# Kernel tuning notes

Measured on AMD Instinct MI355X. Metric: run time of the kernel, lower is better.

## Reference

```python
import jax, jax.numpy as jnp
import numpy as np

N_USERS = 100000
N_ITEMS = 50000
N_EDGES = 1000000
D = 64


def setup_inputs() -> dict:
    key = jax.random.key(0)
    ks = jax.random.split(key, 8)
    return {
        "h_user": jax.random.normal(ks[0], (N_USERS, D), dtype=jnp.float32),
        "h_item": jax.random.normal(ks[1], (N_ITEMS, D), dtype=jnp.float32),
        "buy_src": jax.random.randint(ks[2], (N_EDGES,), 0, N_USERS),
        "buy_dst": jax.random.randint(ks[3], (N_EDGES,), 0, N_ITEMS),
        "w_buy": jax.random.uniform(ks[4], (N_EDGES,), dtype=jnp.float32),
        "bought_src": jax.random.randint(ks[5], (N_EDGES,), 0, N_ITEMS),
        "bought_dst": jax.random.randint(ks[6], (N_EDGES,), 0, N_USERS),
        "w_bought": jax.random.uniform(ks[7], (N_EDGES,), dtype=jnp.float32),
    }


def reference(h_user, h_item, buy_src, buy_dst, w_buy, bought_src, bought_dst, w_bought):
    # 'buy' etype: user -> item. message m = h_user[src] * w, reduce sum at item dst.
    msg_buy = h_user[buy_src] * w_buy[:, None]  # [E, D]
    new_item = jax.ops.segment_sum(msg_buy, buy_dst, num_segments=h_item.shape[0])
    # 'bought' etype: item -> user. message m = h_item[src] * w, reduce sum at user dst.
    msg_bought = h_item[bought_src] * w_bought[:, None]  # [E, D]
    new_user = jax.ops.segment_sum(msg_bought, bought_dst, num_segments=h_user.shape[0])
    # multi_update_all cross-reducer 'mean' is identity here: each ntype is written
    # by exactly one etype, so mean over one contribution == the sum itself.
    return (new_user, new_item)
```

## Files before the change

kernel.cpp:

```cpp
#include <hip/hip_runtime.h>


#define DIM 64

#define RB2     64
#define CAP_I   2048
#define CAP_U   1024
#define NBLK_FC 256

#define RB   128
#define CAP  4096
#define NBLK 256

__global__ void zero_u32(unsigned* __restrict__ p, int n) {
    int i = blockIdx.x * blockDim.x + threadIdx.x;
    if (i < n) p[i] = 0u;
}

__global__ void zero_f32(float4* __restrict__ out, long long n4) {
    long long i = (long long)blockIdx.x * blockDim.x + threadIdx.x;
    const long long stride = (long long)gridDim.x * blockDim.x;
    for (; i < n4; i += stride) out[i] = make_float4(0.f, 0.f, 0.f, 0.f);
}

__global__ void conv_bf16(const float4* __restrict__ in, uint4* __restrict__ out,
                          long long n8) {
    long long i = (long long)blockIdx.x * blockDim.x + threadIdx.x;
    const long long stride = (long long)gridDim.x * blockDim.x;
    for (; i < n8; i += stride) {
        const float4 a = in[2 * i];
        const float4 b = in[2 * i + 1];
        const unsigned* pa = (const unsigned*)&a;
        const unsigned* pb = (const unsigned*)&b;
        unsigned r[8];
        #pragma unroll
        for (int k = 0; k < 4; ++k) {
            unsigned u = pa[k];
            r[k] = (u + 0x7FFFu + ((u >> 16) & 1u)) >> 16;
        }
        #pragma unroll
        for (int k = 0; k < 4; ++k) {
            unsigned u = pb[k];
            r[4 + k] = (u + 0x7FFFu + ((u >> 16) & 1u)) >> 16;
        }
        uint4 o;
        o.x = r[0] | (r[1] << 16);
        o.y = r[2] | (r[3] << 16);
        o.z = r[4] | (r[5] << 16);
        o.w = r[6] | (r[7] << 16);
        out[i] = o;
    }
}

__global__ void scatter_both(const float* __restrict__ h_user,
                             const float* __restrict__ h_item,
                             const int* __restrict__ buy_src,
                             const int* __restrict__ buy_dst,
                             const float* __restrict__ w_buy,
                             const int* __restrict__ bought_src,
                             const int* __restrict__ bought_dst,
                             const float* __restrict__ w_bought,
                             float* __restrict__ new_user,
                             float* __restrict__ new_item,
                             int n_buy, int n_total) {
    const int lane = threadIdx.x & 63;
    const int waves_per_block = blockDim.x >> 6;
    int wid = blockIdx.x * waves_per_block + (threadIdx.x >> 6);
    const int nwaves = gridDim.x * waves_per_block;
    for (int e = wid; e < n_total; e += nwaves) {
        const float* h; const int* srcp; const int* dstp; const float* wp;
        float* outp; int idx;
        if (e < n_buy) { h = h_user; srcp = buy_src; dstp = buy_dst; wp = w_buy; outp = new_item; idx = e; }
        else { h = h_item; srcp = bought_src; dstp = bought_dst; wp = w_bought; outp = new_user; idx = e - n_buy; }
        const int s = srcp[idx];
        const int d = dstp[idx];
        const float weight = wp[idx];
        const float v = h[(long long)s * DIM + lane] * weight;
        atomicAdd(outp + (long long)d * DIM + lane, v);
    }
}


__global__ __launch_bounds__(512) void k3_fc(
        const int* __restrict__ buy_src, const int* __restrict__ buy_dst,
        const float* __restrict__ w_buy,
        const int* __restrict__ bought_src, const int* __restrict__ bought_dst,
        const float* __restrict__ w_bought,
        unsigned* __restrict__ cur, uint2* __restrict__ pay,
        int n_buy, int n_total, int g_item, int G, int chunk) {
    extern __shared__ unsigned sh[];
    for (int g = threadIdx.x; g < G; g += blockDim.x) sh[g] = 0u;
    __syncthreads();
    const int start = blockIdx.x * chunk;
    const int end = (start + chunk < n_total) ? start + chunk : n_total;
    const int step = blockDim.x;

    int i = start + threadIdx.x;
    for (; i + 7 * step < end; i += 8 * step) {
        int g[8];
        #pragma unroll
        for (int u = 0; u < 8; ++u) {
            const int ii = i + u * step;
            g[u] = (ii < n_buy) ? (buy_dst[ii] >> 6)
                                : (g_item + (bought_dst[ii - n_buy] >> 6));
        }
        #pragma unroll
        for (int u = 0; u < 8; ++u) atomicAdd(&sh[g[u]], 1u);
    }
    for (; i < end; i += step) {
        const int g = (i < n_buy) ? (buy_dst[i] >> 6)
                                  : (g_item + (bought_dst[i - n_buy] >> 6));
        atomicAdd(&sh[g], 1u);
    }
    __syncthreads();

    for (int g = threadIdx.x; g < G; g += blockDim.x) {
        const unsigned c = sh[g];
        sh[g] = c ? atomicAdd(&cur[g], c) : 0u;
    }
    __syncthreads();

    i = start + threadIdx.x;
    for (; i + 3 * step < end; i += 4 * step) {
        int srcv[4], dstv[4]; float wv[4]; int g[4];
        #pragma unroll
        for (int u = 0; u < 4; ++u) {
            const int ii = i + u * step;
            if (ii < n_buy) {
                srcv[u] = buy_src[ii]; dstv[u] = buy_dst[ii]; wv[u] = w_buy[ii];
                g[u] = dstv[u] >> 6;
            } else {
                const int j = ii - n_buy;
                srcv[u] = bought_src[j]; dstv[u] = bought_dst[j]; wv[u] = w_bought[j];
                g[u] = g_item + (dstv[u] >> 6);
            }
        }
        #pragma unroll
        for (int u = 0; u < 4; ++u) {
            const unsigned p = atomicAdd(&sh[g[u]], 1u);
            size_t base; unsigned cap;
            if (g[u] < g_item) { base = (size_t)g[u] * CAP_I; cap = CAP_I; }
            else { base = (size_t)g_item * CAP_I + (size_t)(g[u] - g_item) * CAP_U; cap = CAP_U; }
            if (p < cap)
                pay[base + p] = make_uint2((unsigned)srcv[u] | ((unsigned)(dstv[u] & (RB2 - 1)) << 17),
                                           __float_as_uint(wv[u]));
        }
    }
    for (; i < end; i += step) {
        int srcv, dstv; float wv; int g;
        if (i < n_buy) {
            srcv = buy_src[i]; dstv = buy_dst[i]; wv = w_buy[i];
            g = dstv >> 6;
        } else {
            const int j = i - n_buy;
            srcv = bought_src[j]; dstv = bought_dst[j]; wv = w_bought[j];
            g = g_item + (dstv >> 6);
        }
        const unsigned p = atomicAdd(&sh[g], 1u);
        size_t base; unsigned cap;
        if (g < g_item) { base = (size_t)g * CAP_I; cap = CAP_I; }
        else { base = (size_t)g_item * CAP_I + (size_t)(g - g_item) * CAP_U; cap = CAP_U; }
        if (p < cap)
            pay[base + p] = make_uint2((unsigned)srcv | ((unsigned)(dstv & (RB2 - 1)) << 17),
                                       __float_as_uint(wv));
    }
}

__device__ __forceinline__ float bf16_to_f32(unsigned u) {
    return __uint_as_float(u << 16);
}

__global__ __launch_bounds__(256, 8) void p4_bf16(
        const unsigned short* __restrict__ hb_user,
        const unsigned short* __restrict__ hb_item,
        const unsigned* __restrict__ cur, const uint2* __restrict__ pay,
        float* __restrict__ new_user, float* __restrict__ new_item,
        int g_item, int n_user_buckets, int ni_per, int nu_per,
        int n_items, int n_users) {
    __shared__ uint2 pbuf[CAP_I];
    __shared__ unsigned cnt[RB2];
    __shared__ unsigned pos[RB2];
    __shared__ unsigned rstart[RB2];

    const int xcd  = blockIdx.x & 7;
    const int slot = blockIdx.x >> 3;
    int g;
    if (xcd < 4) {
        if (slot >= ni_per) return;
        g = xcd * ni_per + slot;
        if (g >= g_item) return;
    } else {
        if (slot >= nu_per) return;
        const int gu = (xcd - 4) * nu_per + slot;
        if (gu >= n_user_buckets) return;
        g = g_item + gu;
    }

    const int lane = threadIdx.x & 63;
    const int wid  = threadIdx.x >> 6;
    const int sub  = lane >> 4;
    const int c4   = lane & 15;

    const unsigned short* hb; float* outp; int r0, nrowsb, cap; size_t pbase;
    if (g < g_item) {
        hb = hb_user; outp = new_item; r0 = g * RB2;
        nrowsb = n_items - r0; if (nrowsb > RB2) nrowsb = RB2;
        pbase = (size_t)g * CAP_I; cap = CAP_I;
    } else {
        const int gu = g - g_item;
        hb = hb_item; outp = new_user; r0 = gu * RB2;
        nrowsb = n_users - r0; if (nrowsb > RB2) nrowsb = RB2;
        pbase = (size_t)g_item * CAP_I + (size_t)gu * CAP_U; cap = CAP_U;
    }
    int m = (int)cur[g]; if (m > cap) m = cap;

    if (threadIdx.x < RB2) cnt[threadIdx.x] = 0u;
    __syncthreads();

    uint2 v[8];
    #pragma unroll
    for (int j = 0; j < 8; ++j) {
        const int t = (int)threadIdx.x + j * 256;
        if (t < m) {
            v[j] = pay[pbase + t];
            atomicAdd(&cnt[v[j].x >> 17], 1u);
        }
    }
    __syncthreads();
    if (wid == 0) {
        const unsigned x = cnt[lane];
        unsigned sc = x;
        #pragma unroll
        for (int d = 1; d < 64; d <<= 1) {
            unsigned u = __shfl_up(sc, d, 64);
            if (lane >= d) sc += u;
        }
        pos[lane]    = sc - x;
        rstart[lane] = sc - x;
    }
    __syncthreads();
    #pragma unroll
    for (int j = 0; j < 8; ++j) {
        const int t = (int)threadIdx.x + j * 256;
        if (t < m) {
            const unsigned q = atomicAdd(&pos[v[j].x >> 17], 1u);
            pbuf[q] = v[j];
        }
    }
    __syncthreads();

    for (int i = 0; i < 16; ++i) {
        const int r = wid * 16 + i;
        unsigned k = rstart[r];
        const unsigned ke = k + cnt[r];
        float4 a = make_float4(0.f, 0.f, 0.f, 0.f);
        for (; k + 8 <= ke; k += 8) {
            const uint2 pA = pbuf[k + sub];
            const uint2 pB = pbuf[k + 4 + sub];
            const ushort4 hA = *(const ushort4*)(hb + (size_t)(pA.x & 0x1FFFFu) * DIM + c4 * 4);
            const ushort4 hB = *(const ushort4*)(hb + (size_t)(pB.x & 0x1FFFFu) * DIM + c4 * 4);
            const float wA = __uint_as_float(pA.y);
            const float wB = __uint_as_float(pB.y);
            a.x += bf16_to_f32(hA.x) * wA; a.y += bf16_to_f32(hA.y) * wA;
            a.z += bf16_to_f32(hA.z) * wA; a.w += bf16_to_f32(hA.w) * wA;
            a.x += bf16_to_f32(hB.x) * wB; a.y += bf16_to_f32(hB.y) * wB;
            a.z += bf16_to_f32(hB.z) * wB; a.w += bf16_to_f32(hB.w) * wB;
        }
        for (; k < ke; k += 4) {
            const unsigned kk = k + (unsigned)sub;
            const uint2 p = pbuf[kk < ke ? kk : (ke - 1)];
            const float wgt = (kk < ke) ? __uint_as_float(p.y) : 0.f;
            const ushort4 hv = *(const ushort4*)(hb + (size_t)(p.x & 0x1FFFFu) * DIM + c4 * 4);
            a.x += bf16_to_f32(hv.x) * wgt; a.y += bf16_to_f32(hv.y) * wgt;
            a.z += bf16_to_f32(hv.z) * wgt; a.w += bf16_to_f32(hv.w) * wgt;
        }
        a.x += __shfl_xor(a.x, 16, 64); a.y += __shfl_xor(a.y, 16, 64);
        a.z += __shfl_xor(a.z, 16, 64); a.w += __shfl_xor(a.w, 16, 64);
        a.x += __shfl_xor(a.x, 32, 64); a.y += __shfl_xor(a.y, 32, 64);
        a.z += __shfl_xor(a.z, 32, 64); a.w += __shfl_xor(a.w, 32, 64);
        if (lane < 16 && r < nrowsb)
            *((float4*)(outp + (size_t)(r0 + r) * DIM) + c4) = a;
    }
}

__global__ __launch_bounds__(512) void k1_hist(const int* __restrict__ buy_dst,
                                               const int* __restrict__ bought_dst,
                                               unsigned* __restrict__ cnt,
                                               int n_buy, int n_total,
                                               int g_item, int G, int chunk) {
    extern __shared__ unsigned lcnt[];
    for (int g = threadIdx.x; g < G; g += blockDim.x) lcnt[g] = 0u;
    __syncthreads();
    const int start = blockIdx.x * chunk;
    const int end = (start + chunk < n_total) ? start + chunk : n_total;
    for (int i = start + threadIdx.x; i < end; i += blockDim.x) {
        const int g = (i < n_buy) ? (buy_dst[i] >> 7)
                                  : (g_item + (bought_dst[i - n_buy] >> 7));
        atomicAdd(&lcnt[g], 1u);
    }
    __syncthreads();
    for (int g = threadIdx.x; g < G; g += blockDim.x) {
        const unsigned c = lcnt[g];
        if (c) atomicAdd(&cnt[g], c);
    }
}

__global__ __launch_bounds__(64) void k2_scan(const unsigned* __restrict__ cnt,
                                              unsigned* __restrict__ starts,
                                              unsigned* __restrict__ cur, int G) {
    const int lane = threadIdx.x;
    unsigned carry = 0;
    for (int base = 0; base < G; base += 64) {
        const int i = base + lane;
        const unsigned x = (i < G) ? cnt[i] : 0u;
        unsigned sc = x;
        #pragma unroll
        for (int d = 1; d < 64; d <<= 1) {
            unsigned u = __shfl_up(sc, d, 64);
            if (lane >= d) sc += u;
        }
        const unsigned tot = __shfl(sc, 63, 64);
        if (i < G) { starts[i] = carry + sc - x; cur[i] = carry + sc - x; }
        carry += tot;
    }
}

__global__ __launch_bounds__(512) void k3_scatter(
        const int* __restrict__ buy_src, const int* __restrict__ buy_dst,
        const float* __restrict__ w_buy,
        const int* __restrict__ bought_src, const int* __restrict__ bought_dst,
        const float* __restrict__ w_bought,
        unsigned* __restrict__ cur, uint2* __restrict__ pay,
        int n_buy, int n_total, int g_item, int G, int chunk) {
    extern __shared__ unsigned sh[];
    for (int g = threadIdx.x; g < G; g += blockDim.x) sh[g] = 0u;
    __syncthreads();
    const int start = blockIdx.x * chunk;
    const int end = (start + chunk < n_total) ? start + chunk : n_total;
    for (int i = start + threadIdx.x; i < end; i += blockDim.x) {
        const int g = (i < n_buy) ? (buy_dst[i] >> 7)
                                  : (g_item + (bought_dst[i - n_buy] >> 7));
        atomicAdd(&sh[g], 1u);
    }
    __syncthreads();
    for (int g = threadIdx.x; g < G; g += blockDim.x) {
        const unsigned c = sh[g];
        sh[g] = c ? atomicAdd(&cur[g], c) : 0u;
    }
    __syncthreads();
    for (int i = start + threadIdx.x; i < end; i += blockDim.x) {
        int srcv, dstv; float wv; int g;
        if (i < n_buy) {
            srcv = buy_src[i]; dstv = buy_dst[i]; wv = w_buy[i];
            g = dstv >> 7;
        } else {
            const int j = i - n_buy;
            srcv = bought_src[j]; dstv = bought_dst[j]; wv = w_bought[j];
            g = g_item + (dstv >> 7);
        }
        const unsigned pos = atomicAdd(&sh[g], 1u);
        pay[pos] = make_uint2((unsigned)srcv | ((unsigned)(dstv & (RB - 1)) << 17),
                              __float_as_uint(wv));
    }
}

__global__ __launch_bounds__(512) void p4_sortreduce(
        const float* __restrict__ h_user, const float* __restrict__ h_item,
        const unsigned* __restrict__ starts, const uint2* __restrict__ pay,
        float* __restrict__ new_user, float* __restrict__ new_item,
        int g_item, int G, int n_items, int n_users, int n_total) {
    __shared__ uint2 pbuf[CAP];
    __shared__ unsigned cnt[RB];
    __shared__ unsigned pos[RB];
    __shared__ unsigned rstart[RB];

    const int g = blockIdx.x;
    const int lane = threadIdx.x & 63;
    const int wid  = threadIdx.x >> 6;

    const float* h; float* outp; int r0, nrows;
    if (g < g_item) { h = h_user; outp = new_item; r0 = g * RB;
                      nrows = (n_items - r0 < RB) ? n_items - r0 : RB; }
    else            { h = h_item; outp = new_user; r0 = (g - g_item) * RB;
                      nrows = (n_users - r0 < RB) ? n_users - r0 : RB; }

    const unsigned base = starts[g];
    const unsigned endp = (g + 1 < G) ? starts[g + 1] : (unsigned)n_total;

    float acc[16];
    #pragma unroll
    for (int i = 0; i < 16; ++i) acc[i] = 0.f;

    for (unsigned cbase = base; cbase < endp; cbase += CAP) {
        const unsigned rem = endp - cbase;
        const int m = (rem < (unsigned)CAP) ? (int)rem : CAP;

        for (int r = threadIdx.x; r < RB; r += blockDim.x) cnt[r] = 0u;
        __syncthreads();
        for (int t = threadIdx.x; t < m; t += blockDim.x) {
            const uint2 p = pay[cbase + t];
            atomicAdd(&cnt[p.x >> 17], 1u);
        }
        __syncthreads();
        if (wid == 0) {
            unsigned carry = 0;
            #pragma unroll
            for (int b = 0; b < RB; b += 64) {
                const unsigned x = cnt[b + lane];
                unsigned sc = x;
                #pragma unroll
                for (int d = 1; d < 64; d <<= 1) {
                    unsigned u = __shfl_up(sc, d, 64);
                    if (lane >= d) sc += u;
                }
                pos[b + lane]    = carry + sc - x;
                rstart[b + lane] = carry + sc - x;
                carry += __shfl(sc, 63, 64);
            }
        }
        __syncthreads();
        for (int t = threadIdx.x; t < m; t += blockDim.x) {
            const uint2 p = pay[cbase + t];
            const unsigned q = atomicAdd(&pos[p.x >> 17], 1u);
            pbuf[q] = p;
        }
        __syncthreads();
        #pragma unroll
        for (int i = 0; i < 16; ++i) {
            const int r = wid * 16 + i;
            unsigned k = rstart[r];
            const unsigned ke = k + cnt[r];
            float a = acc[i];
            for (; k + 4 <= ke; k += 4) {
                const uint2 p0 = pbuf[k + 0];
                const uint2 p1 = pbuf[k + 1];
                const uint2 p2 = pbuf[k + 2];
                const uint2 p3 = pbuf[k + 3];
                const float v0 = h[(size_t)(p0.x & 0x1FFFFu) * DIM + lane];
                const float v1 = h[(size_t)(p1.x & 0x1FFFFu) * DIM + lane];
                const float v2 = h[(size_t)(p2.x & 0x1FFFFu) * DIM + lane];
                const float v3 = h[(size_t)(p3.x & 0x1FFFFu) * DIM + lane];
                a += v0 * __uint_as_float(p0.y);
                a += v1 * __uint_as_float(p1.y);
                a += v2 * __uint_as_float(p2.y);
                a += v3 * __uint_as_float(p3.y);
            }
            for (; k < ke; ++k) {
                const uint2 p = pbuf[k];
                a += h[(size_t)(p.x & 0x1FFFFu) * DIM + lane] * __uint_as_float(p.y);
            }
            acc[i] = a;
        }
        __syncthreads();
    }

    #pragma unroll
    for (int i = 0; i < 16; ++i) {
        const int r = wid * 16 + i;
        if (r < nrows) outp[(size_t)(r0 + r) * DIM + lane] = acc[i];
    }
}

extern "C" void kernel_launch(void* const* d_in, const int* in_sizes, int n_in,
                              void* d_out, int out_size, void* d_ws, size_t ws_size,
                              hipStream_t stream) {
    const float* h_user     = (const float*)d_in[0];
    const float* h_item     = (const float*)d_in[1];
    const int*   buy_src    = (const int*)d_in[2];
    const int*   buy_dst    = (const int*)d_in[3];
    const float* w_buy      = (const float*)d_in[4];
    const int*   bought_src = (const int*)d_in[5];
    const int*   bought_dst = (const int*)d_in[6];
    const float* w_bought   = (const float*)d_in[7];

    const int n_users  = in_sizes[0] / DIM;
    const int n_items  = in_sizes[1] / DIM;
    const int n_buy    = in_sizes[2];
    const int n_bought = in_sizes[5];
    const int n_total  = n_buy + n_bought;

    float* out      = (float*)d_out;
    float* new_user = out;
    float* new_item = out + (long long)n_users * DIM;

    char* w = (char*)d_ws;
    size_t used = 0;
    auto alloc = [&](size_t bytes) -> char* {
        char* p = w + used;
        used += (bytes + 255) & ~(size_t)255;
        return p;
    };

    {
        const int G_ITEM = (n_items + RB2 - 1) / RB2;
        const int G_USER = (n_users + RB2 - 1) / RB2;
        const int G      = G_ITEM + G_USER;
        const size_t pay_slots = (size_t)G_ITEM * CAP_I + (size_t)G_USER * CAP_U;
        used = 0;
        unsigned*       cur = (unsigned*)alloc((size_t)G * 4);
        uint2*          pay = (uint2*)alloc(pay_slots * 8);
        unsigned short* hb  = (unsigned short*)alloc((size_t)(n_users + n_items) * DIM * 2);
        if (used <= ws_size) {
            unsigned short* hb_user = hb;
            unsigned short* hb_item = hb + (size_t)n_users * DIM;
            const int chunk = (n_total + NBLK_FC - 1) / NBLK_FC;
            const size_t smem_g = (size_t)G * 4;

            const long long n8_user = (long long)n_users * DIM / 8;
            const long long n8_item = (long long)n_items * DIM / 8;
            conv_bf16<<<2048, 256, 0, stream>>>((const float4*)h_user,
                                                (uint4*)hb_user, n8_user);
            conv_bf16<<<1024, 256, 0, stream>>>((const float4*)h_item,
                                                (uint4*)hb_item, n8_item);

            zero_u32<<<(G + 255) / 256, 256, 0, stream>>>(cur, G);
            k3_fc<<<NBLK_FC, 512, smem_g, stream>>>(buy_src, buy_dst, w_buy,
                                                    bought_src, bought_dst, w_bought,
                                                    cur, pay,
                                                    n_buy, n_total, G_ITEM, G, chunk);
            const int ni_per = (G_ITEM + 3) / 4;
            const int nu_per = (G_USER + 3) / 4;
            const int maxper = (ni_per > nu_per) ? ni_per : nu_per;
            const int grid   = 8 * maxper;
            p4_bf16<<<grid, 256, 0, stream>>>(hb_user, hb_item, cur, pay,
                                              new_user, new_item,
                                              G_ITEM, G_USER, ni_per, nu_per,
                                              n_items, n_users);
            return;
        }
    }

    {
        const int G_ITEM = (n_items + RB - 1) / RB;
        const int G_USER = (n_users + RB - 1) / RB;
        const int G      = G_ITEM + G_USER;
        used = 0;
        unsigned* cnt    = (unsigned*)alloc((size_t)G * 4);
        unsigned* starts = (unsigned*)alloc((size_t)G * 4);
        unsigned* cur    = (unsigned*)alloc((size_t)G * 4);
        uint2*    pay    = (uint2*)alloc((size_t)n_total * 8);
        if (used <= ws_size) {
            const int chunk = (n_total + NBLK - 1) / NBLK;
            const size_t smem_g = (size_t)G * 4;
            zero_u32<<<(G + 255) / 256, 256, 0, stream>>>(cnt, G);
            k1_hist<<<NBLK, 512, smem_g, stream>>>(buy_dst, bought_dst, cnt,
                                                   n_buy, n_total, G_ITEM, G, chunk);
            k2_scan<<<1, 64, 0, stream>>>(cnt, starts, cur, G);
            k3_scatter<<<NBLK, 512, smem_g, stream>>>(buy_src, buy_dst, w_buy,
                                                      bought_src, bought_dst, w_bought,
                                                      cur, pay,
                                                      n_buy, n_total, G_ITEM, G, chunk);
            p4_sortreduce<<<G, 512, 0, stream>>>(h_user, h_item, starts, pay,
                                                 new_user, new_item,
                                                 G_ITEM, G, n_items, n_users, n_total);
            return;
        }
    }

    const long long n4 = (long long)out_size / 4;
    zero_f32<<<2048, 256, 0, stream>>>((float4*)d_out, n4);
    scatter_both<<<2048, 256, 0, stream>>>(h_user, h_item,
                                           buy_src, buy_dst, w_buy,
                                           bought_src, bought_dst, w_bought,
                                           new_user, new_item,
                                           n_buy, n_total);
}
```

Measured before the change: 92.66 us.

## Replace global atomic bucket reservation with count matrix and column prefix scan

The fused bin-and-scatter kernel is split into three kernels. The first counts edges per bucket per block into a 16-bit count matrix. The second does a wave-level exclusive scan per bucket row to get each block's offset and the bucket total. The third scatters payloads using those precomputed offsets. This removes the per-block global atomicAdds on bucket cursors and makes the layout deterministic, at the cost of two extra launches, a G×256 matrix round trip through memory, and 16-bit counts that could overflow when a bucket is large.

```diff
diff --git a/kernel.cpp b/kernel.cpp
--- a/kernel.cpp
+++ b/kernel.cpp
@@ -6,7 +6,7 @@
 #define RB2     64
 #define CAP_I   2048
 #define CAP_U   1024
-#define NBLK_FC 256
+#define NBM     256
 
 #define RB   128
 #define CAP  4096
@@ -81,46 +81,82 @@
 }
 
 
-__global__ __launch_bounds__(512) void k3_fc(
+__global__ __launch_bounds__(512) void p1m(
+        const int* __restrict__ buy_dst, const int* __restrict__ bought_dst,
+        unsigned short* __restrict__ cnt_m,
+        int n_buy, int n_total, int g_item, int G, int chunk) {
+    extern __shared__ unsigned sh[];
+    for (int g = threadIdx.x; g < G; g += blockDim.x) sh[g] = 0u;
+    __syncthreads();
+    const int b = blockIdx.x;
+    const int start = b * chunk;
+    const int end = (start + chunk < n_total) ? start + chunk : n_total;
+    const int step = blockDim.x;
+    int i = start + threadIdx.x;
+    for (; i + 7 * step < end; i += 8 * step) {
+        int g[8];
+        #pragma unroll
+        for (int u = 0; u < 8; ++u) {
+            const int ii = i + u * step;
+            g[u] = (ii < n_buy) ? (buy_dst[ii] >> 6)
+                                : (g_item + (bought_dst[ii - n_buy] >> 6));
+        }
+        #pragma unroll
+        for (int u = 0; u < 8; ++u) atomicAdd(&sh[g[u]], 1u);
+    }
+    for (; i < end; i += step) {
+        const int g = (i < n_buy) ? (buy_dst[i] >> 6)
+                                  : (g_item + (bought_dst[i - n_buy] >> 6));
+        atomicAdd(&sh[g], 1u);
+    }
+    __syncthreads();
+    for (int g = threadIdx.x; g < G; g += blockDim.x) {
+        const unsigned c = sh[g];
+        cnt_m[(size_t)g * NBM + b] = (unsigned short)(c > 0xFFFFu ? 0xFFFFu : c);
+    }
+}
+
+__global__ __launch_bounds__(256) void s_col(
+        unsigned short* __restrict__ cnt_m, unsigned* __restrict__ cur, int G) {
+    const int g = blockIdx.x * 4 + ((int)threadIdx.x >> 6);
+    if (g >= G) return;
+    const int lane = threadIdx.x & 63;
+    ushort4* row4 = (ushort4*)(cnt_m + (size_t)g * NBM);
+    const ushort4 v = row4[lane];
+    const unsigned s0 = v.x, s1 = v.y, s2 = v.z, s3 = v.w;
+    const unsigned t = s0 + s1 + s2 + s3;
+    unsigned sc = t;
+    #pragma unroll
+    for (int d = 1; d < 64; d <<= 1) {
+        unsigned u = __shfl_up(sc, d, 64);
+        if (lane >= d) sc += u;
+    }
+    const unsigned excl = sc - t;
+    ushort4 o;
+    o.x = (unsigned short)excl;
+    o.y = (unsigned short)(excl + s0);
+    o.z = (unsigned short)(excl + s0 + s1);
+    o.w = (unsigned short)(excl + s0 + s1 + s2);
+    row4[lane] = o;
+    if (lane == 63) cur[g] = sc;
+}
+
+__global__ __launch_bounds__(512) void p3m(
         const int* __restrict__ buy_src, const int* __restrict__ buy_dst,
         const float* __restrict__ w_buy,
         const int* __restrict__ bought_src, const int* __restrict__ bought_dst,
         const float* __restrict__ w_bought,
-        unsigned* __restrict__ cur, uint2* __restrict__ pay,
+        const unsigned short* __restrict__ cnt_m, uint2* __restrict__ pay,
         int n_buy, int n_total, int g_item, int G, int chunk) {
     extern __shared__ unsigned sh[];
-    for (int g = threadIdx.x; g < G; g += blockDim.x) sh[g] = 0u;
-    __syncthreads();
-    const int start = blockIdx.x * chunk;
+    const int b = blockIdx.x;
+    for (int g = threadIdx.x; g < G; g += blockDim.x)
+        sh[g] = cnt_m[(size_t)g * NBM + b];
+    __syncthreads();
+    const int start = b * chunk;
     const int end = (start + chunk < n_total) ? start + chunk : n_total;
     const int step = blockDim.x;
-
     int i = start + threadIdx.x;
-    for (; i + 7 * step < end; i += 8 * step) {
-        int g[8];
-        #pragma unroll
-        for (int u = 0; u < 8; ++u) {
-            const int ii = i + u * step;
-            g[u] = (ii < n_buy) ? (buy_dst[ii] >> 6)
-                                : (g_item + (bought_dst[ii - n_buy] >> 6));
-        }
-        #pragma unroll
-        for (int u = 0; u < 8; ++u) atomicAdd(&sh[g[u]], 1u);
-    }
-    for (; i < end; i += step) {
-        const int g = (i < n_buy) ? (buy_dst[i] >> 6)
-                                  : (g_item + (bought_dst[i - n_buy] >> 6));
-        atomicAdd(&sh[g], 1u);
-    }
-    __syncthreads();
-
-    for (int g = threadIdx.x; g < G; g += blockDim.x) {
-        const unsigned c = sh[g];
-        sh[g] = c ? atomicAdd(&cur[g], c) : 0u;
-    }
-    __syncthreads();
-
-    i = start + threadIdx.x;
     for (; i + 3 * step < end; i += 4 * step) {
         int srcv[4], dstv[4]; float wv[4]; int g[4];
         #pragma unroll
@@ -497,13 +533,14 @@
         const int G      = G_ITEM + G_USER;
         const size_t pay_slots = (size_t)G_ITEM * CAP_I + (size_t)G_USER * CAP_U;
         used = 0;
-        unsigned*       cur = (unsigned*)alloc((size_t)G * 4);
-        uint2*          pay = (uint2*)alloc(pay_slots * 8);
-        unsigned short* hb  = (unsigned short*)alloc((size_t)(n_users + n_items) * DIM * 2);
+        unsigned*       cur   = (unsigned*)alloc((size_t)G * 4);
+        unsigned short* cnt_m = (unsigned short*)alloc((size_t)G * NBM * 2);
+        uint2*          pay   = (uint2*)alloc(pay_slots * 8);
+        unsigned short* hb    = (unsigned short*)alloc((size_t)(n_users + n_items) * DIM * 2);
         if (used <= ws_size) {
             unsigned short* hb_user = hb;
             unsigned short* hb_item = hb + (size_t)n_users * DIM;
-            const int chunk = (n_total + NBLK_FC - 1) / NBLK_FC;
+            const int chunk = (n_total + NBM - 1) / NBM;
             const size_t smem_g = (size_t)G * 4;
 
             const long long n8_user = (long long)n_users * DIM / 8;
@@ -513,11 +550,14 @@
             conv_bf16<<<1024, 256, 0, stream>>>((const float4*)h_item,
                                                 (uint4*)hb_item, n8_item);
 
-            zero_u32<<<(G + 255) / 256, 256, 0, stream>>>(cur, G);
-            k3_fc<<<NBLK_FC, 512, smem_g, stream>>>(buy_src, buy_dst, w_buy,
-                                                    bought_src, bought_dst, w_bought,
-                                                    cur, pay,
-                                                    n_buy, n_total, G_ITEM, G, chunk);
+            p1m<<<NBM, 512, smem_g, stream>>>(buy_dst, bought_dst, cnt_m,
+                                              n_buy, n_total, G_ITEM, G, chunk);
+            s_col<<<(G + 3) / 4, 256, 0, stream>>>(cnt_m, cur, G);
+            p3m<<<NBM, 512, smem_g, stream>>>(buy_src, buy_dst, w_buy,
+                                              bought_src, bought_dst, w_bought,
+                                              cnt_m, pay,
+                                              n_buy, n_total, G_ITEM, G, chunk);
+
             const int ni_per = (G_ITEM + 3) / 4;
             const int nu_per = (G_USER + 3) / 4;
             const int maxper = (ni_per > nu_per) ? ni_per : nu_per;
```

After: 101.5 us. 9.5% more time.

## Shard bucket cursors across eight sub-buffers to cut global atomic contention

Applied to the files above, without the earlier changes.

Each destination bucket's global cursor and payload region is split into eight shards, with the fill blocks choosing a shard by block index. The aim is to spread the global atomicAdd traffic on the cursors across more addresses so blocks contend less. The consumer kernel now walks eight sub-ranges instead of one contiguous range, and it reads the payload twice from global memory rather than holding it in registers. Per-shard capacities are smaller, which risks overflow (dropped edges) when a bucket's edges land unevenly across shards.

```diff
diff --git a/kernel.cpp b/kernel.cpp
--- a/kernel.cpp
+++ b/kernel.cpp
@@ -4,8 +4,11 @@
 #define DIM 64
 
 #define RB2     64
-#define CAP_I   2048
-#define CAP_U   1024
+#define SH      8
+#define SCAP_I  256
+#define SCAP_U  128
+#define CAP_I   (SH * SCAP_I)
+#define CAP_U   (SH * SCAP_U)
 #define NBLK_FC 256
 
 #define RB   128
@@ -91,7 +94,9 @@
     extern __shared__ unsigned sh[];
     for (int g = threadIdx.x; g < G; g += blockDim.x) sh[g] = 0u;
     __syncthreads();
-    const int start = blockIdx.x * chunk;
+    const int b = blockIdx.x;
+    const int shard = b & (SH - 1);
+    const int start = b * chunk;
     const int end = (start + chunk < n_total) ? start + chunk : n_total;
     const int step = blockDim.x;
 
@@ -116,7 +121,7 @@
 
     for (int g = threadIdx.x; g < G; g += blockDim.x) {
         const unsigned c = sh[g];
-        sh[g] = c ? atomicAdd(&cur[g], c) : 0u;
+        sh[g] = c ? atomicAdd(&cur[(size_t)g * SH + shard], c) : 0u;
     }
     __syncthreads();
 
@@ -138,12 +143,13 @@
         #pragma unroll
         for (int u = 0; u < 4; ++u) {
             const unsigned p = atomicAdd(&sh[g[u]], 1u);
-            size_t base; unsigned cap;
-            if (g[u] < g_item) { base = (size_t)g[u] * CAP_I; cap = CAP_I; }
-            else { base = (size_t)g_item * CAP_I + (size_t)(g[u] - g_item) * CAP_U; cap = CAP_U; }
-            if (p < cap)
-                pay[base + p] = make_uint2((unsigned)srcv[u] | ((unsigned)(dstv[u] & (RB2 - 1)) << 17),
-                                           __float_as_uint(wv[u]));
+            size_t base; unsigned scap;
+            if (g[u] < g_item) { base = (size_t)g[u] * CAP_I; scap = SCAP_I; }
+            else { base = (size_t)g_item * CAP_I + (size_t)(g[u] - g_item) * CAP_U; scap = SCAP_U; }
+            if (p < scap)
+                pay[base + (size_t)shard * scap + p] =
+                    make_uint2((unsigned)srcv[u] | ((unsigned)(dstv[u] & (RB2 - 1)) << 17),
+                               __float_as_uint(wv[u]));
         }
     }
     for (; i < end; i += step) {
@@ -157,12 +163,13 @@
             g = g_item + (dstv >> 6);
         }
         const unsigned p = atomicAdd(&sh[g], 1u);
-        size_t base; unsigned cap;
-        if (g < g_item) { base = (size_t)g * CAP_I; cap = CAP_I; }
-        else { base = (size_t)g_item * CAP_I + (size_t)(g - g_item) * CAP_U; cap = CAP_U; }
-        if (p < cap)
-            pay[base + p] = make_uint2((unsigned)srcv | ((unsigned)(dstv & (RB2 - 1)) << 17),
-                                       __float_as_uint(wv));
+        size_t base; unsigned scap;
+        if (g < g_item) { base = (size_t)g * CAP_I; scap = SCAP_I; }
+        else { base = (size_t)g_item * CAP_I + (size_t)(g - g_item) * CAP_U; scap = SCAP_U; }
+        if (p < scap)
+            pay[base + (size_t)shard * scap + p] =
+                make_uint2((unsigned)srcv | ((unsigned)(dstv & (RB2 - 1)) << 17),
+                           __float_as_uint(wv));
     }
 }
 
@@ -201,30 +208,34 @@
     const int sub  = lane >> 4;
     const int c4   = lane & 15;
 
-    const unsigned short* hb; float* outp; int r0, nrowsb, cap; size_t pbase;
+    const unsigned short* hb; float* outp; int r0, nrowsb; unsigned scap; size_t pbase;
     if (g < g_item) {
         hb = hb_user; outp = new_item; r0 = g * RB2;
         nrowsb = n_items - r0; if (nrowsb > RB2) nrowsb = RB2;
-        pbase = (size_t)g * CAP_I; cap = CAP_I;
+        pbase = (size_t)g * CAP_I; scap = SCAP_I;
     } else {
         const int gu = g - g_item;
         hb = hb_item; outp = new_user; r0 = gu * RB2;
         nrowsb = n_users - r0; if (nrowsb > RB2) nrowsb = RB2;
-        pbase = (size_t)g_item * CAP_I + (size_t)gu * CAP_U; cap = CAP_U;
-    }
-    int m = (int)cur[g]; if (m > cap) m = cap;
+        pbase = (size_t)g_item * CAP_I + (size_t)gu * CAP_U; scap = SCAP_U;
+    }
+
+    unsigned msa[SH];
+    #pragma unroll
+    for (int s = 0; s < SH; ++s) {
+        unsigned c = cur[(size_t)g * SH + s];
+        msa[s] = (c > scap) ? scap : c;
+    }
 
     if (threadIdx.x < RB2) cnt[threadIdx.x] = 0u;
     __syncthreads();
 
-    uint2 v[8];
     #pragma unroll
-    for (int j = 0; j < 8; ++j) {
-        const int t = (int)threadIdx.x + j * 256;
-        if (t < m) {
-            v[j] = pay[pbase + t];
-            atomicAdd(&cnt[v[j].x >> 17], 1u);
-        }
+    for (int s = 0; s < SH; ++s) {
+        const uint2* ps = pay + pbase + (size_t)s * scap;
+        const int ms = (int)msa[s];
+        for (int t = (int)threadIdx.x; t < ms; t += 256)
+            atomicAdd(&cnt[ps[t].x >> 17], 1u);
     }
     __syncthreads();
     if (wid == 0) {
@@ -240,11 +251,13 @@
     }
     __syncthreads();
     #pragma unroll
-    for (int j = 0; j < 8; ++j) {
-        const int t = (int)threadIdx.x + j * 256;
-        if (t < m) {
-            const unsigned q = atomicAdd(&pos[v[j].x >> 17], 1u);
-            pbuf[q] = v[j];
+    for (int s = 0; s < SH; ++s) {
+        const uint2* ps = pay + pbase + (size_t)s * scap;
+        const int ms = (int)msa[s];
+        for (int t = (int)threadIdx.x; t < ms; t += 256) {
+            const uint2 p = ps[t];
+            const unsigned q = atomicAdd(&pos[p.x >> 17], 1u);
+            pbuf[q] = p;
         }
     }
     __syncthreads();
@@ -497,7 +510,7 @@
         const int G      = G_ITEM + G_USER;
         const size_t pay_slots = (size_t)G_ITEM * CAP_I + (size_t)G_USER * CAP_U;
         used = 0;
-        unsigned*       cur = (unsigned*)alloc((size_t)G * 4);
+        unsigned*       cur = (unsigned*)alloc((size_t)G * SH * 4);
         uint2*          pay = (uint2*)alloc(pay_slots * 8);
         unsigned short* hb  = (unsigned short*)alloc((size_t)(n_users + n_items) * DIM * 2);
         if (used <= ws_size) {
@@ -513,11 +526,12 @@
             conv_bf16<<<1024, 256, 0, stream>>>((const float4*)h_item,
                                                 (uint4*)hb_item, n8_item);
 
-            zero_u32<<<(G + 255) / 256, 256, 0, stream>>>(cur, G);
+            zero_u32<<<(G * SH + 255) / 256, 256, 0, stream>>>(cur, G * SH);
             k3_fc<<<NBLK_FC, 512, smem_g, stream>>>(buy_src, buy_dst, w_buy,
                                                     bought_src, bought_dst, w_bought,
                                                     cur, pay,
                                                     n_buy, n_total, G_ITEM, G, chunk);
+
             const int ni_per = (G_ITEM + 3) / 4;
             const int nu_per = (G_USER + 3) / 4;
             const int maxper = (ni_per > nu_per) ? ni_per : nu_per;
```

After: 99.52 us. 7.4% more time.
